# Optimization experiments

Hardware: AMD Instinct MI355X
Metric: run time of the kernel (lower is better)

## Reference

```python
import jax, jax.numpy as jnp
import numpy as np

TOP_K = 1


def _mlp(x, gw, uw, dw):
    # SwiGLU MLP: down( silu(x @ gate.T) * (x @ up.T) )
    return (jax.nn.silu(x @ gw.T) * (x @ uw.T)) @ dw.T


def setup_inputs() -> dict:
    key = jax.random.key(0)
    ks = jax.random.split(key, 8)
    B, S, H, I, E = 2, 1024, 2048, 4096, 8
    s = 0.02  # weight scale for numerical sanity
    return {
        "hidden_states": jax.random.normal(ks[0], (B, S, H), jnp.float32),
        "router_w": jax.random.normal(ks[1], (E, H), jnp.float32) * s,
        "shared_gate_w": jax.random.normal(ks[2], (I, H), jnp.float32) * s,
        "shared_up_w": jax.random.normal(ks[3], (I, H), jnp.float32) * s,
        "shared_down_w": jax.random.normal(ks[4], (H, I), jnp.float32) * s,
        "exp_gate_w": jax.random.normal(ks[5], (E, I, H), jnp.float32) * s,
        "exp_up_w": jax.random.normal(ks[6], (E, I, H), jnp.float32) * s,
        "exp_down_w": jax.random.normal(ks[7], (E, H, I), jnp.float32) * s,
    }


def reference(hidden_states, router_w, shared_gate_w, shared_up_w, shared_down_w,
              exp_gate_w, exp_up_w, exp_down_w):
    B, S, H = hidden_states.shape
    E = router_w.shape[0]
    hs = hidden_states.reshape(-1, H)              # [T, H]
    T = hs.shape[0]
    logits = hs @ router_w.T                       # [T, E]
    top_val, top_idx = jax.lax.top_k(logits, TOP_K)
    masked = jnp.full_like(logits, -jnp.inf).at[jnp.arange(T)[:, None], top_idx].set(top_val)
    router_scores = jax.nn.sigmoid(masked.astype(jnp.float32)).T.astype(hs.dtype)  # [E, T]
    # Literal torch semantics: routed_in = tile(hs, (E,1)) * router_scores.reshape(-1,1),
    # and the loop consumes only rows 0..E-1 (routed_in[i:i+1, :]).
    # Row i (i < T since E << T) = hs[i] * router_scores[0, i].
    rows = hs[:E] * router_scores.reshape(-1)[:E, None]        # [E, H]
    gate = jnp.einsum('eh,eih->ei', rows, exp_gate_w)          # [E, I]
    up = jnp.einsum('eh,eih->ei', rows, exp_up_w)              # [E, I]
    expert_out = jnp.einsum('ei,ehi->eh', jax.nn.silu(gate) * up, exp_down_w)  # [E, H]
    # out += experts[i](routed_in[i:i+1]) broadcasts each [1,H] over all T rows.
    out = _mlp(hs, shared_gate_w, shared_up_w, shared_down_w) + expert_out.sum(axis=0)
    return out, router_scores
```

## Files before the change

### kernel.cpp

```cpp
#include <hip/hip_runtime.h>
#include <math.h>

typedef __attribute__((ext_vector_type(8))) short short8_t;
typedef __attribute__((ext_vector_type(4))) float f32x4;

__device__ __forceinline__ short f2bf(float f) {
  unsigned u = __builtin_bit_cast(unsigned, f);
  u = (u + 0x7fffu + ((u >> 16) & 1u)) >> 16;
  return (short)u;
}
__device__ __forceinline__ float sigmoid_f(float x) { return 1.f / (1.f + expf(-x)); }
__device__ __forceinline__ float silu_f(float x)    { return x / (1.f + expf(-x)); }

__global__ __launch_bounds__(256) void router_kernel(
    const float* __restrict__ hs, const float* __restrict__ rw,
    float* __restrict__ scores, float* __restrict__ scale, int T, int H) {
  const int wave = threadIdx.x >> 6, lane = threadIdx.x & 63;
  const int t = blockIdx.x * 4 + wave;
  if (t >= T) return;
  float acc[8] = {0.f,0.f,0.f,0.f,0.f,0.f,0.f,0.f};
  for (int h = lane * 4; h < H; h += 256) {
    const float4 x = *(const float4*)(hs + (size_t)t * H + h);
#pragma unroll
    for (int e = 0; e < 8; ++e) {
      const float4 wv = *(const float4*)(rw + (size_t)e * H + h);
      acc[e] += x.x*wv.x + x.y*wv.y + x.z*wv.z + x.w*wv.w;
    }
  }
#pragma unroll
  for (int e = 0; e < 8; ++e)
#pragma unroll
    for (int off = 32; off > 0; off >>= 1)
      acc[e] += __shfl_xor(acc[e], off, 64);
  if (lane == 0) {
    int amax = 0; float best = acc[0];
#pragma unroll
    for (int e = 1; e < 8; ++e) if (acc[e] > best) { best = acc[e]; amax = e; }
#pragma unroll
    for (int e = 0; e < 8; ++e)
      scores[(size_t)e * T + t] = (e == amax) ? sigmoid_f(acc[e]) : 0.f;
    if (t < 8) scale[t] = (amax == 0) ? sigmoid_f(acc[0]) : 0.f;
  }
}

__global__ __launch_bounds__(256) void expert_gateup_kernel(
    const float* __restrict__ hs, const float* __restrict__ gw,
    const float* __restrict__ uw, const float* __restrict__ scale,
    float* __restrict__ act, int H, int I) {
  const int e = blockIdx.y;
  const float s = scale[e];
  if (s == 0.f) return;
  const int wave = threadIdx.x >> 6, lane = threadIdx.x & 63;
  const float* hrow = hs + (size_t)e * H;
#pragma unroll
  for (int j = 0; j < 4; ++j) {
    const int i = blockIdx.x * 16 + j * 4 + wave;
    const float* grow = gw + ((size_t)e * I + i) * H;
    const float* urow = uw + ((size_t)e * I + i) * H;
    float pg = 0.f, pu = 0.f;
    for (int h = lane * 4; h < H; h += 256) {
      const float4 x  = *(const float4*)(hrow + h);
      const float4 g4 = *(const float4*)(grow + h);
      const float4 u4 = *(const float4*)(urow + h);
      pg += x.x*g4.x + x.y*g4.y + x.z*g4.z + x.w*g4.w;
      pu += x.x*u4.x + x.y*u4.y + x.z*u4.z + x.w*u4.w;
    }
#pragma unroll
    for (int off = 32; off > 0; off >>= 1) {
      pg += __shfl_xor(pg, off, 64);
      pu += __shfl_xor(pu, off, 64);
    }
    if (lane == 0) {
      const float g = s * pg, u = s * pu;
      act[(size_t)e * I + i] = silu_f(g) * u;
    }
  }
}

__global__ __launch_bounds__(256) void expert_down_kernel(
    const float* __restrict__ act, const float* __restrict__ dw,
    const float* __restrict__ scale, float* __restrict__ bias, int H, int I) {
  const int e = blockIdx.y;
  if (scale[e] == 0.f) return;
  const int wave = threadIdx.x >> 6, lane = threadIdx.x & 63;
  const int h = blockIdx.x * 4 + wave;
  const float* drow = dw + ((size_t)e * H + h) * I;
  const float* arow = act + (size_t)e * I;
  float p = 0.f;
  for (int i = lane * 4; i < I; i += 256) {
    const float4 a = *(const float4*)(arow + i);
    const float4 d = *(const float4*)(drow + i);
    p += a.x*d.x + a.y*d.y + a.z*d.z + a.w*d.w;
  }
#pragma unroll
  for (int off = 32; off > 0; off >>= 1) p += __shfl_xor(p, off, 64);
  if (lane == 0) atomicAdd(bias + h, p);
}

__device__ __forceinline__ void stage_f32_tile(short* __restrict__ dst,
                                               const float* __restrict__ src,
                                               int ldk, int tid) {
  const int r = tid >> 3;
  const int c = (tid & 7) << 2;
#pragma unroll
  for (int it = 0; it < 4; ++it) {
    const float4 v = *(const float4*)(src + (size_t)(r + it * 32) * ldk + c);
    short4 hv;
    hv.x = f2bf(v.x); hv.y = f2bf(v.y); hv.z = f2bf(v.z); hv.w = f2bf(v.w);
    *(short4*)(dst + (r + it * 32) * 32 + c) = hv;
  }
}
__device__ __forceinline__ void stage_bf16_tile(short* __restrict__ dst,
                                                const short* __restrict__ src,
                                                int ldk, int tid) {
  const int r = tid >> 2;
  const int c = (tid & 3) << 3;
#pragma unroll
  for (int it = 0; it < 2; ++it) {
    const int4 v = *(const int4*)(src + (size_t)(r + it * 64) * ldk + c);
    *(int4*)(dst + (r + it * 64) * 32 + c) = v;
  }
}

__global__ __launch_bounds__(256) void gemm_gateup_kernel(
    const float* __restrict__ X, const float* __restrict__ Wg,
    const float* __restrict__ Wu, short* __restrict__ Act,
    int M, int N, int K) {
  __shared__ short As[128 * 32];
  __shared__ short Bgs[128 * 32];
  __shared__ short Bus[128 * 32];
  const int tid = threadIdx.x;
  const int lane = tid & 63, wave = tid >> 6;
  const int wm = wave & 1, wn = wave >> 1;
  const int m0 = blockIdx.x * 128, n0 = blockIdx.y * 128;
  const f32x4 vzero = {0.f, 0.f, 0.f, 0.f};
  f32x4 accg[4][4], accu[4][4];
#pragma unroll
  for (int mi = 0; mi < 4; ++mi)
#pragma unroll
    for (int ni = 0; ni < 4; ++ni) { accg[mi][ni] = vzero; accu[mi][ni] = vzero; }
  const float* Ap  = X  + (size_t)m0 * K;
  const float* Bgp = Wg + (size_t)n0 * K;
  const float* Bup = Wu + (size_t)n0 * K;
  const int row = lane & 15, q = lane >> 4;
  for (int k0 = 0; k0 < K; k0 += 32) {
    stage_f32_tile(As,  Ap  + k0, K, tid);
    stage_f32_tile(Bgs, Bgp + k0, K, tid);
    stage_f32_tile(Bus, Bup + k0, K, tid);
    __syncthreads();
    short8_t a[4], bg[4], bu[4];
#pragma unroll
    for (int i = 0; i < 4; ++i) {
      a[i]  = *(const short8_t*)(As  + (wm * 64 + i * 16 + row) * 32 + q * 8);
      bg[i] = *(const short8_t*)(Bgs + (wn * 64 + i * 16 + row) * 32 + q * 8);
      bu[i] = *(const short8_t*)(Bus + (wn * 64 + i * 16 + row) * 32 + q * 8);
    }
#pragma unroll
    for (int mi = 0; mi < 4; ++mi)
#pragma unroll
      for (int ni = 0; ni < 4; ++ni) {
        accg[mi][ni] = __builtin_amdgcn_mfma_f32_16x16x32_bf16(a[mi], bg[ni], accg[mi][ni], 0, 0, 0);
        accu[mi][ni] = __builtin_amdgcn_mfma_f32_16x16x32_bf16(a[mi], bu[ni], accu[mi][ni], 0, 0, 0);
      }
    __syncthreads();
  }
  const int col = lane & 15, rb = (lane >> 4) * 4;
#pragma unroll
  for (int mi = 0; mi < 4; ++mi)
#pragma unroll
    for (int ni = 0; ni < 4; ++ni)
#pragma unroll
      for (int r = 0; r < 4; ++r) {
        const int gm = m0 + wm * 64 + mi * 16 + rb + r;
        const int gn = n0 + wn * 64 + ni * 16 + col;
        const float g = accg[mi][ni][r];
        const float u = accu[mi][ni][r];
        Act[(size_t)gm * N + gn] = f2bf(silu_f(g) * u);
      }
}

__global__ __launch_bounds__(256) void gemm_down_kernel(
    const short* __restrict__ Aact, const float* __restrict__ Wd,
    const float* __restrict__ bias, float* __restrict__ Out,
    int M, int N, int K) {
  __shared__ short As[128 * 32];
  __shared__ short Bs[128 * 32];
  const int tid = threadIdx.x;
  const int lane = tid & 63, wave = tid >> 6;
  const int wm = wave & 1, wn = wave >> 1;
  const int m0 = blockIdx.x * 128, n0 = blockIdx.y * 128;
  const f32x4 vzero = {0.f, 0.f, 0.f, 0.f};
  f32x4 acc[4][4];
#pragma unroll
  for (int mi = 0; mi < 4; ++mi)
#pragma unroll
    for (int ni = 0; ni < 4; ++ni) acc[mi][ni] = vzero;
  const short* Ap = Aact + (size_t)m0 * K;
  const float* Bp = Wd + (size_t)n0 * K;
  const int row = lane & 15, q = lane >> 4;
  for (int k0 = 0; k0 < K; k0 += 32) {
    stage_bf16_tile(As, Ap + k0, K, tid);
    stage_f32_tile(Bs, Bp + k0, K, tid);
    __syncthreads();
    short8_t a[4], b[4];
#pragma unroll
    for (int i = 0; i < 4; ++i) {
      a[i] = *(const short8_t*)(As + (wm * 64 + i * 16 + row) * 32 + q * 8);
      b[i] = *(const short8_t*)(Bs + (wn * 64 + i * 16 + row) * 32 + q * 8);
    }
#pragma unroll
    for (int mi = 0; mi < 4; ++mi)
#pragma unroll
      for (int ni = 0; ni < 4; ++ni)
        acc[mi][ni] = __builtin_amdgcn_mfma_f32_16x16x32_bf16(a[mi], b[ni], acc[mi][ni], 0, 0, 0);
    __syncthreads();
  }
  const int col = lane & 15, rb = (lane >> 4) * 4;
#pragma unroll
  for (int mi = 0; mi < 4; ++mi)
#pragma unroll
    for (int ni = 0; ni < 4; ++ni)
#pragma unroll
      for (int r = 0; r < 4; ++r) {
        const int gm = m0 + wm * 64 + mi * 16 + rb + r;
        const int gn = n0 + wn * 64 + ni * 16 + col;
        Out[(size_t)gm * N + gn] = acc[mi][ni][r] + bias[gn];
      }
}

extern "C" void kernel_launch(void* const* d_in, const int* in_sizes, int n_in,
                              void* d_out, int out_size, void* d_ws, size_t ws_size,
                              hipStream_t stream) {
  const float* hs  = (const float*)d_in[0];
  const float* rw  = (const float*)d_in[1];
  const float* sgw = (const float*)d_in[2];
  const float* suw = (const float*)d_in[3];
  const float* sdw = (const float*)d_in[4];
  const float* egw = (const float*)d_in[5];
  const float* euw = (const float*)d_in[6];
  const float* edw = (const float*)d_in[7];

  const int E = in_sizes[5] / in_sizes[2];
  const int H = in_sizes[1] / E;
  const int I = in_sizes[2] / H;
  const int T = in_sizes[0] / H;

  float* out    = (float*)d_out;
  float* scores = out + (size_t)T * H;

  char* w = (char*)d_ws;
  float* scale = (float*)w;  w += 256;
  float* bias  = (float*)w;  w += ((size_t)H * 4 + 255) & ~(size_t)255;
  float* act   = (float*)w;  w += ((size_t)E * I * 4 + 255) & ~(size_t)255;
  short* Aact  = (short*)w;

  router_kernel<<<dim3(T / 4), 256, 0, stream>>>(hs, rw, scores, scale, T, H);
  hipMemsetAsync(bias, 0, (size_t)H * sizeof(float), stream);
  expert_gateup_kernel<<<dim3(I / 16, E), 256, 0, stream>>>(hs, egw, euw, scale, act, H, I);
  expert_down_kernel<<<dim3(H / 4, E), 256, 0, stream>>>(act, edw, scale, bias, H, I);
  gemm_gateup_kernel<<<dim3(T / 128, I / 128), 256, 0, stream>>>(hs, sgw, suw, Aact, T, I, H);
  gemm_down_kernel<<<dim3(T / 128, H / 128), 256, 0, stream>>>(Aact, sdw, bias, out, T, H, I);
}
```

Before: 961.0 us.

## Pre-convert shared MLP operands to bf16 and stage tiles via direct global-to-LDS loads

Adds a conversion pass that casts hidden states and the shared gate/up/down weights to bf16 in workspace before the GEMMs. The GEMM kernels then load 16-byte chunks straight into LDS with global_load_lds instead of reading fp32, converting in registers and writing to LDS. An XOR swizzle on the k-chunk index is meant to reduce LDS bank conflicts on the fragment reads. This halves GEMM operand bytes and removes the in-loop conversion work, but adds an extra read/write pass over roughly 100MB of fp32 data each call.

```diff
diff --git a/kernel.cpp b/kernel.cpp
--- a/kernel.cpp
+++ b/kernel.cpp
@@ -3,6 +3,7 @@
 
 typedef __attribute__((ext_vector_type(8))) short short8_t;
 typedef __attribute__((ext_vector_type(4))) float f32x4;
+typedef unsigned int u32;
 
 __device__ __forceinline__ short f2bf(float f) {
   unsigned u = __builtin_bit_cast(unsigned, f);
@@ -11,6 +12,24 @@
 }
 __device__ __forceinline__ float sigmoid_f(float x) { return 1.f / (1.f + expf(-x)); }
 __device__ __forceinline__ float silu_f(float x)    { return x / (1.f + expf(-x)); }
+
+__device__ __forceinline__ void gload_lds16(const void* g, void* l) {
+  __builtin_amdgcn_global_load_lds(
+      (const __attribute__((address_space(1))) u32*)g,
+      (__attribute__((address_space(3))) u32*)l, 16, 0, 0);
+}
+
+__global__ __launch_bounds__(256) void cvt_bf16_kernel(
+    const float* __restrict__ src, short* __restrict__ dst, int n) {
+  const int i = (blockIdx.x * 256 + threadIdx.x) * 8;
+  if (i >= n) return;
+  const float4 v0 = *(const float4*)(src + i);
+  const float4 v1 = *(const float4*)(src + i + 4);
+  short8_t o;
+  o[0] = f2bf(v0.x); o[1] = f2bf(v0.y); o[2] = f2bf(v0.z); o[3] = f2bf(v0.w);
+  o[4] = f2bf(v1.x); o[5] = f2bf(v1.y); o[6] = f2bf(v1.z); o[7] = f2bf(v1.w);
+  *(short8_t*)(dst + i) = o;
+}
 
 __global__ __launch_bounds__(256) void router_kernel(
     const float* __restrict__ hs, const float* __restrict__ rw,
@@ -70,10 +89,7 @@
       pg += __shfl_xor(pg, off, 64);
       pu += __shfl_xor(pu, off, 64);
     }
-    if (lane == 0) {
-      const float g = s * pg, u = s * pu;
-      act[(size_t)e * I + i] = silu_f(g) * u;
-    }
+    if (lane == 0) act[(size_t)e * I + i] = silu_f(s * pg) * (s * pu);
   }
 }
 
@@ -97,63 +113,49 @@
   if (lane == 0) atomicAdd(bias + h, p);
 }
 
-__device__ __forceinline__ void stage_f32_tile(short* __restrict__ dst,
-                                               const float* __restrict__ src,
-                                               int ldk, int tid) {
-  const int r = tid >> 3;
-  const int c = (tid & 7) << 2;
-#pragma unroll
-  for (int it = 0; it < 4; ++it) {
-    const float4 v = *(const float4*)(src + (size_t)(r + it * 32) * ldk + c);
-    short4 hv;
-    hv.x = f2bf(v.x); hv.y = f2bf(v.y); hv.z = f2bf(v.z); hv.w = f2bf(v.w);
-    *(short4*)(dst + (r + it * 32) * 32 + c) = hv;
-  }
-}
-__device__ __forceinline__ void stage_bf16_tile(short* __restrict__ dst,
-                                                const short* __restrict__ src,
-                                                int ldk, int tid) {
-  const int r = tid >> 2;
-  const int c = (tid & 3) << 3;
-#pragma unroll
-  for (int it = 0; it < 2; ++it) {
-    const int4 v = *(const int4*)(src + (size_t)(r + it * 64) * ldk + c);
-    *(int4*)(dst + (r + it * 64) * 32 + c) = v;
-  }
-}
 
 __global__ __launch_bounds__(256) void gemm_gateup_kernel(
-    const float* __restrict__ X, const float* __restrict__ Wg,
-    const float* __restrict__ Wu, short* __restrict__ Act,
+    const short* __restrict__ X, const short* __restrict__ Wg,
+    const short* __restrict__ Wu, short* __restrict__ Act,
     int M, int N, int K) {
   __shared__ short As[128 * 32];
   __shared__ short Bgs[128 * 32];
   __shared__ short Bus[128 * 32];
-  const int tid = threadIdx.x;
-  const int lane = tid & 63, wave = tid >> 6;
+  const int tid = threadIdx.x, lane = tid & 63, wave = tid >> 6;
   const int wm = wave & 1, wn = wave >> 1;
   const int m0 = blockIdx.x * 128, n0 = blockIdx.y * 128;
-  const f32x4 vzero = {0.f, 0.f, 0.f, 0.f};
+
+  const int srow = tid >> 2;
+  const int schunk = (tid & 3) ^ ((tid >> 3) & 3);
+  const size_t a0 = (size_t)(m0 + srow) * K + schunk * 8;
+  const size_t a1 = (size_t)(m0 + 64 + srow) * K + schunk * 8;
+  const size_t b0 = (size_t)(n0 + srow) * K + schunk * 8;
+  const size_t b1 = (size_t)(n0 + 64 + srow) * K + schunk * 8;
+  short* lA0 = As + tid * 8;          short* lA1 = As + 2048 + tid * 8;
+  short* lG0 = Bgs + tid * 8;         short* lG1 = Bgs + 2048 + tid * 8;
+  short* lU0 = Bus + tid * 8;         short* lU1 = Bus + 2048 + tid * 8;
+
+  const f32x4 vz = {0.f,0.f,0.f,0.f};
   f32x4 accg[4][4], accu[4][4];
 #pragma unroll
   for (int mi = 0; mi < 4; ++mi)
 #pragma unroll
-    for (int ni = 0; ni < 4; ++ni) { accg[mi][ni] = vzero; accu[mi][ni] = vzero; }
-  const float* Ap  = X  + (size_t)m0 * K;
-  const float* Bgp = Wg + (size_t)n0 * K;
-  const float* Bup = Wu + (size_t)n0 * K;
-  const int row = lane & 15, q = lane >> 4;
+    for (int ni = 0; ni < 4; ++ni) { accg[mi][ni] = vz; accu[mi][ni] = vz; }
+
+  const int row16 = lane & 15, q = lane >> 4;
+  const int koff = (q ^ ((row16 >> 1) & 3)) * 8;
+
   for (int k0 = 0; k0 < K; k0 += 32) {
-    stage_f32_tile(As,  Ap  + k0, K, tid);
-    stage_f32_tile(Bgs, Bgp + k0, K, tid);
-    stage_f32_tile(Bus, Bup + k0, K, tid);
+    gload_lds16(X + a0 + k0, lA0);  gload_lds16(X + a1 + k0, lA1);
+    gload_lds16(Wg + b0 + k0, lG0); gload_lds16(Wg + b1 + k0, lG1);
+    gload_lds16(Wu + b0 + k0, lU0); gload_lds16(Wu + b1 + k0, lU1);
     __syncthreads();
     short8_t a[4], bg[4], bu[4];
 #pragma unroll
     for (int i = 0; i < 4; ++i) {
-      a[i]  = *(const short8_t*)(As  + (wm * 64 + i * 16 + row) * 32 + q * 8);
-      bg[i] = *(const short8_t*)(Bgs + (wn * 64 + i * 16 + row) * 32 + q * 8);
-      bu[i] = *(const short8_t*)(Bus + (wn * 64 + i * 16 + row) * 32 + q * 8);
+      a[i]  = *(const short8_t*)(As  + (wm * 64 + i * 16 + row16) * 32 + koff);
+      bg[i] = *(const short8_t*)(Bgs + (wn * 64 + i * 16 + row16) * 32 + koff);
+      bu[i] = *(const short8_t*)(Bus + (wn * 64 + i * 16 + row16) * 32 + koff);
     }
 #pragma unroll
     for (int mi = 0; mi < 4; ++mi)
@@ -173,40 +175,47 @@
       for (int r = 0; r < 4; ++r) {
         const int gm = m0 + wm * 64 + mi * 16 + rb + r;
         const int gn = n0 + wn * 64 + ni * 16 + col;
-        const float g = accg[mi][ni][r];
-        const float u = accu[mi][ni][r];
-        Act[(size_t)gm * N + gn] = f2bf(silu_f(g) * u);
+        Act[(size_t)gm * N + gn] = f2bf(silu_f(accg[mi][ni][r]) * accu[mi][ni][r]);
       }
 }
 
 __global__ __launch_bounds__(256) void gemm_down_kernel(
-    const short* __restrict__ Aact, const float* __restrict__ Wd,
+    const short* __restrict__ Aact, const short* __restrict__ Wd,
     const float* __restrict__ bias, float* __restrict__ Out,
     int M, int N, int K) {
   __shared__ short As[128 * 32];
   __shared__ short Bs[128 * 32];
-  const int tid = threadIdx.x;
-  const int lane = tid & 63, wave = tid >> 6;
+  const int tid = threadIdx.x, lane = tid & 63, wave = tid >> 6;
   const int wm = wave & 1, wn = wave >> 1;
   const int m0 = blockIdx.x * 128, n0 = blockIdx.y * 128;
-  const f32x4 vzero = {0.f, 0.f, 0.f, 0.f};
+  const int srow = tid >> 2;
+  const int schunk = (tid & 3) ^ ((tid >> 3) & 3);
+  const size_t a0 = (size_t)(m0 + srow) * K + schunk * 8;
+  const size_t a1 = (size_t)(m0 + 64 + srow) * K + schunk * 8;
+  const size_t b0 = (size_t)(n0 + srow) * K + schunk * 8;
+  const size_t b1 = (size_t)(n0 + 64 + srow) * K + schunk * 8;
+  short* lA0 = As + tid * 8;  short* lA1 = As + 2048 + tid * 8;
+  short* lB0 = Bs + tid * 8;  short* lB1 = Bs + 2048 + tid * 8;
+
+  const f32x4 vz = {0.f,0.f,0.f,0.f};
   f32x4 acc[4][4];
 #pragma unroll
   for (int mi = 0; mi < 4; ++mi)
 #pragma unroll
-    for (int ni = 0; ni < 4; ++ni) acc[mi][ni] = vzero;
-  const short* Ap = Aact + (size_t)m0 * K;
-  const float* Bp = Wd + (size_t)n0 * K;
-  const int row = lane & 15, q = lane >> 4;
+    for (int ni = 0; ni < 4; ++ni) acc[mi][ni] = vz;
+
+  const int row16 = lane & 15, q = lane >> 4;
+  const int koff = (q ^ ((row16 >> 1) & 3)) * 8;
+
   for (int k0 = 0; k0 < K; k0 += 32) {
-    stage_bf16_tile(As, Ap + k0, K, tid);
-    stage_f32_tile(Bs, Bp + k0, K, tid);
+    gload_lds16(Aact + a0 + k0, lA0); gload_lds16(Aact + a1 + k0, lA1);
+    gload_lds16(Wd + b0 + k0, lB0);   gload_lds16(Wd + b1 + k0, lB1);
     __syncthreads();
     short8_t a[4], b[4];
 #pragma unroll
     for (int i = 0; i < 4; ++i) {
-      a[i] = *(const short8_t*)(As + (wm * 64 + i * 16 + row) * 32 + q * 8);
-      b[i] = *(const short8_t*)(Bs + (wn * 64 + i * 16 + row) * 32 + q * 8);
+      a[i] = *(const short8_t*)(As + (wm * 64 + i * 16 + row16) * 32 + koff);
+      b[i] = *(const short8_t*)(Bs + (wn * 64 + i * 16 + row16) * 32 + koff);
     }
 #pragma unroll
     for (int mi = 0; mi < 4; ++mi)
@@ -252,12 +261,24 @@
   float* scale = (float*)w;  w += 256;
   float* bias  = (float*)w;  w += ((size_t)H * 4 + 255) & ~(size_t)255;
   float* act   = (float*)w;  w += ((size_t)E * I * 4 + 255) & ~(size_t)255;
+  short* hsb   = (short*)w;  w += ((size_t)T * H * 2 + 255) & ~(size_t)255;
+  short* gb    = (short*)w;  w += ((size_t)I * H * 2 + 255) & ~(size_t)255;
+  short* ub    = (short*)w;  w += ((size_t)I * H * 2 + 255) & ~(size_t)255;
+  short* db    = (short*)w;  w += ((size_t)H * I * 2 + 255) & ~(size_t)255;
   short* Aact  = (short*)w;
 
   router_kernel<<<dim3(T / 4), 256, 0, stream>>>(hs, rw, scores, scale, T, H);
   hipMemsetAsync(bias, 0, (size_t)H * sizeof(float), stream);
+
+  const int nTH = T * H, nIH = I * H;
+  cvt_bf16_kernel<<<dim3(nTH / 2048), 256, 0, stream>>>(hs, hsb, nTH);
+  cvt_bf16_kernel<<<dim3(nIH / 2048), 256, 0, stream>>>(sgw, gb, nIH);
+  cvt_bf16_kernel<<<dim3(nIH / 2048), 256, 0, stream>>>(suw, ub, nIH);
+  cvt_bf16_kernel<<<dim3(nIH / 2048), 256, 0, stream>>>(sdw, db, nIH);
+
   expert_gateup_kernel<<<dim3(I / 16, E), 256, 0, stream>>>(hs, egw, euw, scale, act, H, I);
   expert_down_kernel<<<dim3(H / 4, E), 256, 0, stream>>>(act, edw, scale, bias, H, I);
-  gemm_gateup_kernel<<<dim3(T / 128, I / 128), 256, 0, stream>>>(hs, sgw, suw, Aact, T, I, H);
-  gemm_down_kernel<<<dim3(T / 128, H / 128), 256, 0, stream>>>(Aact, sdw, bias, out, T, H, I);
-}
+
+  gemm_gateup_kernel<<<dim3(T / 128, I / 128), 256, 0, stream>>>(hsb, gb, ub, Aact, T, I, H);
+  gemm_down_kernel<<<dim3(T / 128, H / 128), 256, 0, stream>>>(Aact, db, bias, out, T, H, I);
+}
```

After: 871.4 us. 9.3% less time.
